# Kernel optimization log

Hardware: AMD Instinct MI355X
Metric: run time of the kernel (lower is better)

## Reference

```python
import jax, jax.numpy as jnp
import numpy as np

B, N, F, T, E, OUT = 16, 5000, 8, 12, 160000, 64


def setup_inputs() -> dict:
    key = jax.random.key(0)
    ks = jax.random.split(key, 20)
    d = {}
    d["x"] = jax.random.normal(ks[0], (B, N, F, T), dtype=jnp.float32)
    d["edge_index"] = jax.random.randint(ks[1], (2, E), 0, N, dtype=jnp.int32)
    def p(k, shape, scale=0.1):
        return jax.random.normal(k, shape, dtype=jnp.float32) * scale
    i = 2
    for g in ("z", "r", "h"):
        d[f"W{g}"] = p(ks[i], (F, OUT)); i += 1        # GCNConv weight
        d[f"b{g}"] = p(ks[i], (OUT,)); i += 1           # GCNConv bias
        d[f"L{g}"] = p(ks[i], (2 * OUT, OUT)); i += 1   # gate Linear weight
        d[f"lb{g}"] = p(ks[i], (OUT,)); i += 1          # gate Linear bias
    d["att"] = p(ks[i], (T,)); i += 1                   # A3TGCN attention logits
    d["fcW"] = p(ks[i], (OUT, T)); i += 1               # final Linear 64->periods
    d["fcb"] = p(ks[i], (T,))
    return d


def _gcn(xs, W, b, src, dst, norm, n_nodes):
    # xs: [M, N, F] -> D^{-1/2}(A+I)D^{-1/2} (xs W) + b
    support = xs @ W                                    # [M, N, OUT]
    msg = support[:, src, :] * norm[None, :, None]      # gather at source
    agg = jax.vmap(lambda m: jax.ops.segment_sum(m, dst, num_segments=n_nodes))(msg)
    return agg + b


def reference(x, edge_index, Wz, bz, Lz, lbz, Wr, br, Lr, lbr, Wh, bh, Lh, lbh, att, fcW, fcb):
    b_sz, n_nodes, _, periods = x.shape
    src, dst = edge_index[0], edge_index[1]
    loop = jnp.arange(n_nodes, dtype=src.dtype)
    src = jnp.concatenate([src, loop])                  # add self loops
    dst = jnp.concatenate([dst, loop])
    deg = jax.ops.segment_sum(jnp.ones(src.shape, jnp.float32), dst, num_segments=n_nodes)
    dinv = jnp.where(deg > 0, jax.lax.rsqrt(deg), 0.0)
    norm = dinv[src] * dinv[dst]                        # symmetric GCN normalization

    # In A3TGCN the hidden state is never carried across periods (stays zero),
    # so all periods are independent: fold T into the batch axis.
    xs = jnp.moveaxis(x, 3, 0).reshape(periods * b_sz, n_nodes, x.shape[2])
    H = jnp.zeros((periods * b_sz, n_nodes, Wz.shape[1]), x.dtype)

    Z = jax.nn.sigmoid(jnp.concatenate([_gcn(xs, Wz, bz, src, dst, norm, n_nodes), H], -1) @ Lz + lbz)
    R = jax.nn.sigmoid(jnp.concatenate([_gcn(xs, Wr, br, src, dst, norm, n_nodes), H], -1) @ Lr + lbr)
    Ht = jnp.tanh(jnp.concatenate([_gcn(xs, Wh, bh, src, dst, norm, n_nodes), H * R], -1) @ Lh + lbh)
    Hnew = Z * H + (1.0 - Z) * Ht                       # [T*B, N, 64]

    Hs = Hnew.reshape(periods, b_sz, n_nodes, -1)
    Hacc = jnp.einsum('t,tbnh->bnh', jax.nn.softmax(att), Hs)
    return Hacc @ fcW + fcb                             # [B, N, periods]
```

## Files before the change

kernel.cpp:

```cpp
#include <hip/hip_runtime.h>

#define NN 5000
#define FF 8
#define TT 12
#define EE 160000
#define HH 64
#define EN (EE + NN)
#define CAP (EN + 7 * NN + 64)
#define XBSTRIDE 1920000
#define BSOFF    15360000

typedef float f2  __attribute__((ext_vector_type(2)));
typedef float f4v __attribute__((ext_vector_type(4)));

#define LOG2E 1.44269504088896340736f


__global__ void k_count(const int* __restrict__ dst, int* __restrict__ deg) {
    int i = blockIdx.x * blockDim.x + threadIdx.x;
    if (i < EE) atomicAdd(&deg[dst[i]], 1);
}

__global__ __launch_bounds__(256) void k_scan_prep(
    const int* __restrict__ deg, int* __restrict__ offs, int* __restrict__ cursor,
    float* __restrict__ dinv,
    const float* __restrict__ Wz, const float* __restrict__ bz,
    const float* __restrict__ Lz, const float* __restrict__ lbz,
    const float* __restrict__ Wh, const float* __restrict__ bh,
    const float* __restrict__ Lh, const float* __restrict__ lbh,
    const float* __restrict__ att,
    float* __restrict__ G, float* __restrict__ C, float* __restrict__ sm) {
    int tid = threadIdx.x;
    if (blockIdx.x == 0) {
        __shared__ int s[256];
        int base = tid * 20;
        int pad[20], real[20];
        int part = 0;
#pragma unroll
        for (int j = 0; j < 20; ++j) {
            int n = base + j;
            int c = (n < NN) ? deg[n] + 1 : 0;
            real[j] = c;
            pad[j] = (c + 7) & ~7;
            part += pad[j];
        }
        s[tid] = part;
        __syncthreads();
        for (int d = 1; d < 256; d <<= 1) {
            int v = (tid >= d) ? s[tid - d] : 0;
            __syncthreads();
            s[tid] += v;
            __syncthreads();
        }
        int run = s[tid] - part;
#pragma unroll
        for (int j = 0; j < 20; ++j) {
            int n = base + j;
            if (n < NN) {
                offs[n] = run;
                cursor[n] = run;
                dinv[n] = rsqrtf((float)real[j]);
                run += pad[j];
            }
        }
        if (tid == 255) offs[NN] = s[255];
    } else {
        for (int idx = tid; idx < 1024; idx += 256) {
            int g = idx >> 9, rem = idx & 511, f = rem >> 6, o = rem & 63;
            const float* W = g ? Wh : Wz;
            const float* L = g ? Lh : Lz;
            float acc = 0.f;
            for (int k = 0; k < 64; ++k) acc += W[f * 64 + k] * L[k * 64 + o];
            G[idx] = acc * (g ? 2.0f * LOG2E : LOG2E);
        }
        for (int idx = tid; idx < 128; idx += 256) {
            int g = idx >> 6, o = idx & 63;
            const float* b = g ? bh : bz;
            const float* L = g ? Lh : Lz;
            const float* lb = g ? lbh : lbz;
            float acc = lb[o];
            for (int k = 0; k < 64; ++k) acc += b[k] * L[k * 64 + o];
            C[idx] = acc * (g ? 2.0f * LOG2E : LOG2E);
        }
        if (tid == 0) {
            float m = att[0];
            for (int t = 1; t < TT; ++t) m = fmaxf(m, att[t]);
            float e[TT], ss = 0.f;
            for (int t = 0; t < TT; ++t) { e[t] = __expf(att[t] - m); ss += e[t]; }
            for (int t = 0; t < TT; ++t) sm[t] = e[t] / ss;
        }
    }
}

__global__ void k_fill(const int* __restrict__ src, const int* __restrict__ dst,
                       int* cursor, const float* __restrict__ dinv,
                       int2* __restrict__ cedge) {
    int i = blockIdx.x * blockDim.x + threadIdx.x;
    if (i < EE) {
        int s = src[i], d = dst[i];
        int p = atomicAdd(&cursor[d], 1);
        cedge[p] = make_int2(s, __float_as_int(dinv[s] * dinv[d]));
    } else if (i < EN) {
        int n = i - EE;
        int p = atomicAdd(&cursor[n], 1);
        cedge[p] = make_int2(n, __float_as_int(dinv[n] * dinv[n]));
    }
}


#define E2(Q)                                                     \
    {                                                             \
        unsigned a0_ = (unsigned)(Q).x * 384u + voff;             \
        unsigned a1_ = (unsigned)(Q).z * 384u + voff;             \
        f4v v0_ = *(const f4v*)(xbb + a0_);                       \
        f4v v1_ = *(const f4v*)(xbb + a1_);                       \
        acc += __int_as_float((Q).y) * v0_;                       \
        acc += __int_as_float((Q).w) * v1_;                       \
    }

__global__ __launch_bounds__(256) void k_fused(
    const float* __restrict__ x, const int* __restrict__ offs,
    const int2* __restrict__ cedge,
    const float* __restrict__ G, const float* __restrict__ C,
    const float* __restrict__ sm, const float* __restrict__ fcW,
    const float* __restrict__ fcb, float* __restrict__ out) {
    __shared__ __align__(16) float xals[4][2][96];
    __shared__ __align__(16) float hl[4][2][72];
    __shared__ __align__(16) float fcw[768];
    __shared__ __align__(16) float Glds[1024];
    __shared__ __align__(16) float Clds[128];

    const int tid = threadIdx.x;
    const int wid = tid >> 6;
    const int lane = tid & 63;
    const int bp = blockIdx.x & 7;
    const int g = blockIdx.x >> 3;
    const int n = g * 4 + wid;

    ((f4v*)Glds)[tid] = ((const f4v*)G)[tid];
    if (tid < 192) ((f4v*)fcw)[tid] = ((const f4v*)fcW)[tid];
    if (tid < 32) ((f4v*)Clds)[tid] = ((const f4v*)C)[tid];

    int r0 = __builtin_amdgcn_readfirstlane(offs[n]);
    int r1 = __builtin_amdgcn_readfirstlane(offs[n + 1]);

    const char* xbb = (const char*)x + (size_t)bp * XBSTRIDE;

    if (lane < 48) {
        const unsigned voff = (unsigned)(lane / 24) * BSOFF + (unsigned)(lane % 24) * 16u;
        f4v acc = {0.f, 0.f, 0.f, 0.f};

        const int4* ce = (const int4*)cedge;
        int c = r0 >> 1;
        const int c1 = r1 >> 1;
        int4 A0 = ce[c], A1 = ce[c + 1], A2 = ce[c + 2], A3 = ce[c + 3];
        int4 B0 = ce[c + 4], B1 = ce[c + 5], B2 = ce[c + 6], B3 = ce[c + 7];
        while (true) {
            int4 D0 = A0, D1 = A1, D2 = A2, D3 = A3;
            A0 = B0; A1 = B1; A2 = B2; A3 = B3;
            B0 = ce[c + 8]; B1 = ce[c + 9]; B2 = ce[c + 10]; B3 = ce[c + 11];
            E2(D0) E2(D1) E2(D2) E2(D3)
            c += 4;
            if (c >= c1) break;
        }
        *(f4v*)&xals[wid][lane / 24][(lane % 24) * 4] = acc;
    }
    __syncthreads();

    float gz[FF], gh[FF];
#pragma unroll
    for (int f = 0; f < FF; ++f) {
        gz[f] = Glds[f * 64 + lane];
        gh[f] = Glds[512 + f * 64 + lane];
    }
    float cz = Clds[lane], ch = Clds[64 + lane];
    float smv[TT];
#pragma unroll
    for (int t = 0; t < TT; ++t) smv[t] = sm[t];

#pragma unroll
    for (int bs = 0; bs < 2; ++bs) {
        float hacc = 0.f;
#pragma unroll
        for (int tq = 0; tq < 3; ++tq) {
            f4v xq[FF];
#pragma unroll
            for (int f = 0; f < FF; ++f)
                xq[f] = *(const f4v*)&xals[wid][bs][f * TT + tq * 4];
#pragma unroll
            for (int half = 0; half < 2; ++half) {
                f2 az = {cz, cz}, ah = {ch, ch};
#pragma unroll
                for (int f = 0; f < FF; ++f) {
                    f2 v = half ? xq[f].hi : xq[f].lo;
                    az += v * gz[f];
                    ah += v * gh[f];
                }
#pragma unroll
                for (int j = 0; j < 2; ++j) {
                    float ea = exp2f(az[j]);
                    float e2h = exp2f(ah[j]);
                    float num = e2h - 1.0f;
                    float den = (1.0f + ea) * (1.0f + e2h);
                    hacc += smv[tq * 4 + half * 2 + j] * num * __builtin_amdgcn_rcpf(den);
                }
            }
        }
        hl[wid][bs][lane] = hacc;
    }
    __syncthreads();

    if (tid < 48) {
        int nw = tid / 12;
        int rem = tid % 12;
        int bs = rem / 6;
        int tp = rem % 6;
        f2 acc;
        acc[0] = fcb[2 * tp];
        acc[1] = fcb[2 * tp + 1];
        const float* hrow = &hl[nw][bs][0];
#pragma unroll
        for (int o4 = 0; o4 < 16; ++o4) {
            f4v h4 = *(const f4v*)&hrow[o4 * 4];
            f2 w0 = *(const f2*)&fcw[(o4 * 4 + 0) * TT + 2 * tp];
            f2 w1 = *(const f2*)&fcw[(o4 * 4 + 1) * TT + 2 * tp];
            f2 w2 = *(const f2*)&fcw[(o4 * 4 + 2) * TT + 2 * tp];
            f2 w3 = *(const f2*)&fcw[(o4 * 4 + 3) * TT + 2 * tp];
            acc += h4[0] * w0;
            acc += h4[1] * w1;
            acc += h4[2] * w2;
            acc += h4[3] * w3;
        }
        int b = bp + bs * 8;
        int nn2 = g * 4 + nw;
        *(f2*)&out[((size_t)b * NN + nn2) * TT + 2 * tp] = acc;
    }
}

extern "C" void kernel_launch(void* const* d_in, const int* in_sizes, int n_in,
                              void* d_out, int out_size, void* d_ws, size_t ws_size,
                              hipStream_t stream) {
    const float* x   = (const float*)d_in[0];
    const int*   ei  = (const int*)d_in[1];
    const float* Wz  = (const float*)d_in[2];
    const float* bz  = (const float*)d_in[3];
    const float* Lz  = (const float*)d_in[4];
    const float* lbz = (const float*)d_in[5];
    const float* Wh  = (const float*)d_in[10];
    const float* bh  = (const float*)d_in[11];
    const float* Lh  = (const float*)d_in[12];
    const float* lbh = (const float*)d_in[13];
    const float* att = (const float*)d_in[14];
    const float* fcW = (const float*)d_in[15];
    const float* fcb = (const float*)d_in[16];
    float* out = (float*)d_out;

    const int* src = ei;
    const int* dst = ei + EE;

    int2*  cedge  = (int2*)d_ws;
    int*   deg    = (int*)(cedge + CAP);
    int*   cursor = deg + NN;
    int*   offs   = cursor + NN;
    float* dinv   = (float*)(offs + NN + 1);
    float* G      = dinv + NN;
    float* C      = G + 1024;
    float* sm     = C + 128;

    (void)hipMemsetAsync(d_ws, 0, (size_t)CAP * 8 + (size_t)NN * 4, stream);
    hipLaunchKernelGGL(k_count, dim3((EE + 255) / 256), dim3(256), 0, stream, dst, deg);
    hipLaunchKernelGGL(k_scan_prep, dim3(2), dim3(256), 0, stream,
                       deg, offs, cursor, dinv,
                       Wz, bz, Lz, lbz, Wh, bh, Lh, lbh, att, G, C, sm);
    hipLaunchKernelGGL(k_fill, dim3((EN + 255) / 256), dim3(256), 0, stream,
                       src, dst, cursor, dinv, cedge);
    hipLaunchKernelGGL(k_fused, dim3(1250 * 8), dim3(256), 0, stream,
                       x, offs, cedge, G, C, sm, fcW, fcb, out);
}
```

Before: 137.5 us.

## Split fused GCN kernel into gather and dense kernels via workspace buffer

```diff
diff --git a/kernel.cpp b/kernel.cpp
--- a/kernel.cpp
+++ b/kernel.cpp
@@ -9,6 +9,7 @@
 #define CAP (EN + 7 * NN + 64)
 #define XBSTRIDE 1920000
 #define BSOFF    15360000
+#define XAFLOATS (8 * NN * 192)
 
 typedef float f2  __attribute__((ext_vector_type(2)));
 typedef float f4v __attribute__((ext_vector_type(4)));
@@ -28,8 +29,9 @@
     const float* __restrict__ Lz, const float* __restrict__ lbz,
     const float* __restrict__ Wh, const float* __restrict__ bh,
     const float* __restrict__ Lh, const float* __restrict__ lbh,
-    const float* __restrict__ att,
-    float* __restrict__ G, float* __restrict__ C, float* __restrict__ sm) {
+    const float* __restrict__ att, const float* __restrict__ fcW,
+    float* __restrict__ G, float* __restrict__ C, float* __restrict__ sm,
+    float* __restrict__ fcwT) {
     int tid = threadIdx.x;
     if (blockIdx.x == 0) {
         __shared__ int s[256];
@@ -81,6 +83,10 @@
             float acc = lb[o];
             for (int k = 0; k < 64; ++k) acc += b[k] * L[k * 64 + o];
             C[idx] = acc * (g ? 2.0f * LOG2E : LOG2E);
+        }
+        for (int idx = tid; idx < 768; idx += 256) {
+            int t = idx >> 6, o = idx & 63;
+            fcwT[idx] = fcW[o * TT + t];
         }
         if (tid == 0) {
             float m = att[0];
@@ -108,6 +114,126 @@
 }
 
 
+#define E2S(Q)                                                    \
+    {                                                             \
+        unsigned a0_ = (unsigned)(Q).x * 384u + voff;             \
+        unsigned a1_ = (unsigned)(Q).z * 384u + voff;             \
+        f4v v0_ = *(const f4v*)(xbb + a0_);                       \
+        f4v v1_ = *(const f4v*)(xbb + a1_);                       \
+        accA += __int_as_float((Q).y) * v0_;                      \
+        accB += __int_as_float((Q).w) * v1_;                      \
+    }
+
+__global__ __launch_bounds__(256) void k_gather(
+    const float* __restrict__ x, const int* __restrict__ offs,
+    const int2* __restrict__ cedge, float* __restrict__ xa) {
+    const int tid = threadIdx.x;
+    const int wid = tid >> 6;
+    const int lane = tid & 63;
+    const int bp = blockIdx.x & 7;
+    const int n = (blockIdx.x >> 3) * 4 + wid;
+
+    int r0 = __builtin_amdgcn_readfirstlane(offs[n]);
+    int r1 = __builtin_amdgcn_readfirstlane(offs[n + 1]);
+
+    const char* xbb = (const char*)x + (size_t)bp * XBSTRIDE;
+
+    if (lane < 48) {
+        const unsigned voff = (unsigned)(lane / 24) * BSOFF + (unsigned)(lane % 24) * 16u;
+        f4v accA = {0.f, 0.f, 0.f, 0.f};
+        f4v accB = {0.f, 0.f, 0.f, 0.f};
+
+        const int4* ce = (const int4*)cedge;
+        int c = r0 >> 1;
+        const int c1 = r1 >> 1;
+        int4 A0 = ce[c], A1 = ce[c + 1], A2 = ce[c + 2], A3 = ce[c + 3];
+        int4 B0 = ce[c + 4], B1 = ce[c + 5], B2 = ce[c + 6], B3 = ce[c + 7];
+        while (true) {
+            int4 D0 = A0, D1 = A1, D2 = A2, D3 = A3;
+            A0 = B0; A1 = B1; A2 = B2; A3 = B3;
+            B0 = ce[c + 8]; B1 = ce[c + 9]; B2 = ce[c + 10]; B3 = ce[c + 11];
+            E2S(D0) E2S(D1) E2S(D2) E2S(D3)
+            c += 4;
+            if (c >= c1) break;
+        }
+        f4v acc = accA + accB;
+        *(f4v*)(xa + ((size_t)(bp * NN + n)) * 192 + (lane / 24) * 96 + (lane % 24) * 4) = acc;
+    }
+}
+
+
+__global__ __launch_bounds__(256) void k_dense(
+    const float* __restrict__ xa, const float* __restrict__ G,
+    const float* __restrict__ C, const float* __restrict__ sm,
+    const float* __restrict__ fcwT, const float* __restrict__ fcb,
+    float* __restrict__ out) {
+    __shared__ __align__(16) float hl[4][128];
+    const int tid = threadIdx.x;
+    const int wid = tid >> 6;
+    const int lane = tid & 63;
+    const int bp = blockIdx.x & 7;
+    const int n = (blockIdx.x >> 3) * 4 + wid;
+
+    const float* row = xa + ((size_t)(bp * NN + n)) * 192;
+
+    float gz[FF], gh[FF];
+#pragma unroll
+    for (int f = 0; f < FF; ++f) {
+        gz[f] = G[f * 64 + lane];
+        gh[f] = G[512 + f * 64 + lane];
+    }
+    float cz = C[lane], ch = C[64 + lane];
+    float smv[TT];
+#pragma unroll
+    for (int t = 0; t < TT; ++t) smv[t] = sm[t];
+
+#pragma unroll
+    for (int bs = 0; bs < 2; ++bs) {
+        float hacc = 0.f;
+#pragma unroll
+        for (int tq = 0; tq < 3; ++tq) {
+            f4v xq[FF];
+#pragma unroll
+            for (int f = 0; f < FF; ++f)
+                xq[f] = *(const f4v*)(row + bs * 96 + f * TT + tq * 4);
+#pragma unroll
+            for (int half = 0; half < 2; ++half) {
+                f2 az = {cz, cz}, ah = {ch, ch};
+#pragma unroll
+                for (int f = 0; f < FF; ++f) {
+                    f2 v = half ? xq[f].hi : xq[f].lo;
+                    az += v * gz[f];
+                    ah += v * gh[f];
+                }
+#pragma unroll
+                for (int j = 0; j < 2; ++j) {
+                    float ea = exp2f(az[j]);
+                    float e2h = exp2f(ah[j]);
+                    float num = e2h - 1.0f;
+                    float den = (1.0f + ea) * (1.0f + e2h);
+                    hacc += smv[tq * 4 + half * 2 + j] * num * __builtin_amdgcn_rcpf(den);
+                }
+            }
+        }
+        hl[wid][bs * 64 + lane] = hacc;
+    }
+    __syncthreads();
+
+    if (lane < 24) {
+        int bs = lane / 12, t = lane % 12;
+        float acc = fcb[t];
+#pragma unroll
+        for (int o4 = 0; o4 < 16; ++o4) {
+            f4v h4 = *(const f4v*)&hl[wid][bs * 64 + o4 * 4];
+            f4v w4 = *(const f4v*)&fcwT[t * 64 + o4 * 4];
+            acc += h4[0] * w4[0] + h4[1] * w4[1] + h4[2] * w4[2] + h4[3] * w4[3];
+        }
+        int b = bp + bs * 8;
+        out[((size_t)b * NN + n) * TT + t] = acc;
+    }
+}
+
+
 #define E2(Q)                                                     \
     {                                                             \
         unsigned a0_ = (unsigned)(Q).x * 384u + voff;             \
@@ -143,13 +269,11 @@
 
     int r0 = __builtin_amdgcn_readfirstlane(offs[n]);
     int r1 = __builtin_amdgcn_readfirstlane(offs[n + 1]);
-
     const char* xbb = (const char*)x + (size_t)bp * XBSTRIDE;
 
     if (lane < 48) {
         const unsigned voff = (unsigned)(lane / 24) * BSOFF + (unsigned)(lane % 24) * 16u;
         f4v acc = {0.f, 0.f, 0.f, 0.f};
-
         const int4* ce = (const int4*)cedge;
         int c = r0 >> 1;
         const int c1 = r1 >> 1;
@@ -258,7 +382,13 @@
     const int* src = ei;
     const int* dst = ei + EE;
 
-    int2*  cedge  = (int2*)d_ws;
+    const size_t need = (size_t)XAFLOATS * 4 + (size_t)CAP * 8 +
+                        (size_t)(3 * NN + 1) * 4 + (size_t)NN * 4 +
+                        (1024 + 128 + 16 + 768) * 4;
+    const bool split = ws_size >= need;
+
+    float* xa     = (float*)d_ws;
+    int2*  cedge  = split ? (int2*)(xa + XAFLOATS) : (int2*)d_ws;
     int*   deg    = (int*)(cedge + CAP);
     int*   cursor = deg + NN;
     int*   offs   = cursor + NN;
@@ -266,14 +396,22 @@
     float* G      = dinv + NN;
     float* C      = G + 1024;
     float* sm     = C + 128;
-
-    (void)hipMemsetAsync(d_ws, 0, (size_t)CAP * 8 + (size_t)NN * 4, stream);
+    float* fcwT   = sm + 16;
+
+    (void)hipMemsetAsync(cedge, 0, (size_t)CAP * 8 + (size_t)NN * 4, stream);
     hipLaunchKernelGGL(k_count, dim3((EE + 255) / 256), dim3(256), 0, stream, dst, deg);
     hipLaunchKernelGGL(k_scan_prep, dim3(2), dim3(256), 0, stream,
                        deg, offs, cursor, dinv,
-                       Wz, bz, Lz, lbz, Wh, bh, Lh, lbh, att, G, C, sm);
+                       Wz, bz, Lz, lbz, Wh, bh, Lh, lbh, att, fcW, G, C, sm, fcwT);
     hipLaunchKernelGGL(k_fill, dim3((EN + 255) / 256), dim3(256), 0, stream,
                        src, dst, cursor, dinv, cedge);
-    hipLaunchKernelGGL(k_fused, dim3(1250 * 8), dim3(256), 0, stream,
-                       x, offs, cedge, G, C, sm, fcW, fcb, out);
-}
+    if (split) {
+        hipLaunchKernelGGL(k_gather, dim3(1250 * 8), dim3(256), 0, stream,
+                           x, offs, cedge, xa);
+        hipLaunchKernelGGL(k_dense, dim3(1250 * 8), dim3(256), 0, stream,
+                           xa, G, C, sm, fcwT, fcb, out);
+    } else {
+        hipLaunchKernelGGL(k_fused, dim3(1250 * 8), dim3(256), 0, stream,
+                           x, offs, cedge, G, C, sm, fcW, fcb, out);
+    }
+}
```

Result: slower. 195.7 us (+42.4%).

## Use one 64-thread block per node, split accumulators, pretranspose fc weights

Applied to the files above, without the earlier changes.

```diff
diff --git a/kernel.cpp b/kernel.cpp
--- a/kernel.cpp
+++ b/kernel.cpp
@@ -21,23 +21,24 @@
     if (i < EE) atomicAdd(&deg[dst[i]], 1);
 }
 
-__global__ __launch_bounds__(256) void k_scan_prep(
+__global__ __launch_bounds__(1024) void k_scan_prep(
     const int* __restrict__ deg, int* __restrict__ offs, int* __restrict__ cursor,
     float* __restrict__ dinv,
     const float* __restrict__ Wz, const float* __restrict__ bz,
     const float* __restrict__ Lz, const float* __restrict__ lbz,
     const float* __restrict__ Wh, const float* __restrict__ bh,
     const float* __restrict__ Lh, const float* __restrict__ lbh,
-    const float* __restrict__ att,
-    float* __restrict__ G, float* __restrict__ C, float* __restrict__ sm) {
+    const float* __restrict__ att, const float* __restrict__ fcW,
+    float* __restrict__ G, float* __restrict__ C, float* __restrict__ sm,
+    float* __restrict__ fcwT) {
     int tid = threadIdx.x;
     if (blockIdx.x == 0) {
-        __shared__ int s[256];
-        int base = tid * 20;
-        int pad[20], real[20];
+        __shared__ int s[1024];
+        int base = tid * 5;
+        int pad[5], real[5];
         int part = 0;
 #pragma unroll
-        for (int j = 0; j < 20; ++j) {
+        for (int j = 0; j < 5; ++j) {
             int n = base + j;
             int c = (n < NN) ? deg[n] + 1 : 0;
             real[j] = c;
@@ -46,7 +47,7 @@
         }
         s[tid] = part;
         __syncthreads();
-        for (int d = 1; d < 256; d <<= 1) {
+        for (int d = 1; d < 1024; d <<= 1) {
             int v = (tid >= d) ? s[tid - d] : 0;
             __syncthreads();
             s[tid] += v;
@@ -54,7 +55,7 @@
         }
         int run = s[tid] - part;
 #pragma unroll
-        for (int j = 0; j < 20; ++j) {
+        for (int j = 0; j < 5; ++j) {
             int n = base + j;
             if (n < NN) {
                 offs[n] = run;
@@ -63,24 +64,28 @@
                 run += pad[j];
             }
         }
-        if (tid == 255) offs[NN] = s[255];
+        if (tid == 1023) offs[NN] = s[1023];
     } else {
-        for (int idx = tid; idx < 1024; idx += 256) {
-            int g = idx >> 9, rem = idx & 511, f = rem >> 6, o = rem & 63;
+        if (tid < 1024) {
+            int g = tid >> 9, rem = tid & 511, f = rem >> 6, o = rem & 63;
             const float* W = g ? Wh : Wz;
             const float* L = g ? Lh : Lz;
             float acc = 0.f;
             for (int k = 0; k < 64; ++k) acc += W[f * 64 + k] * L[k * 64 + o];
-            G[idx] = acc * (g ? 2.0f * LOG2E : LOG2E);
-        }
-        for (int idx = tid; idx < 128; idx += 256) {
-            int g = idx >> 6, o = idx & 63;
+            G[tid] = acc * (g ? 2.0f * LOG2E : LOG2E);
+        }
+        if (tid < 128) {
+            int g = tid >> 6, o = tid & 63;
             const float* b = g ? bh : bz;
             const float* L = g ? Lh : Lz;
             const float* lb = g ? lbh : lbz;
             float acc = lb[o];
             for (int k = 0; k < 64; ++k) acc += b[k] * L[k * 64 + o];
-            C[idx] = acc * (g ? 2.0f * LOG2E : LOG2E);
+            C[tid] = acc * (g ? 2.0f * LOG2E : LOG2E);
+        }
+        if (tid < 768) {
+            int t = tid >> 6, o = tid & 63;
+            fcwT[tid] = fcW[o * TT + t];
         }
         if (tid == 0) {
             float m = att[0];
@@ -108,38 +113,28 @@
 }
 
 
-#define E2(Q)                                                     \
+#define E2S(Q)                                                    \
     {                                                             \
         unsigned a0_ = (unsigned)(Q).x * 384u + voff;             \
         unsigned a1_ = (unsigned)(Q).z * 384u + voff;             \
         f4v v0_ = *(const f4v*)(xbb + a0_);                       \
         f4v v1_ = *(const f4v*)(xbb + a1_);                       \
-        acc += __int_as_float((Q).y) * v0_;                       \
-        acc += __int_as_float((Q).w) * v1_;                       \
-    }
-
-__global__ __launch_bounds__(256) void k_fused(
+        accA += __int_as_float((Q).y) * v0_;                      \
+        accB += __int_as_float((Q).w) * v1_;                      \
+    }
+
+__global__ __launch_bounds__(64) void k_node(
     const float* __restrict__ x, const int* __restrict__ offs,
     const int2* __restrict__ cedge,
     const float* __restrict__ G, const float* __restrict__ C,
-    const float* __restrict__ sm, const float* __restrict__ fcW,
+    const float* __restrict__ sm, const float* __restrict__ fcwT,
     const float* __restrict__ fcb, float* __restrict__ out) {
-    __shared__ __align__(16) float xals[4][2][96];
-    __shared__ __align__(16) float hl[4][2][72];
-    __shared__ __align__(16) float fcw[768];
-    __shared__ __align__(16) float Glds[1024];
-    __shared__ __align__(16) float Clds[128];
-
-    const int tid = threadIdx.x;
-    const int wid = tid >> 6;
-    const int lane = tid & 63;
+    __shared__ __align__(16) float xals[2][96];
+    __shared__ __align__(16) float hl[2][64];
+
+    const int lane = threadIdx.x;
     const int bp = blockIdx.x & 7;
-    const int g = blockIdx.x >> 3;
-    const int n = g * 4 + wid;
-
-    ((f4v*)Glds)[tid] = ((const f4v*)G)[tid];
-    if (tid < 192) ((f4v*)fcw)[tid] = ((const f4v*)fcW)[tid];
-    if (tid < 32) ((f4v*)Clds)[tid] = ((const f4v*)C)[tid];
+    const int n = blockIdx.x >> 3;
 
     int r0 = __builtin_amdgcn_readfirstlane(offs[n]);
     int r1 = __builtin_amdgcn_readfirstlane(offs[n + 1]);
@@ -148,7 +143,8 @@
 
     if (lane < 48) {
         const unsigned voff = (unsigned)(lane / 24) * BSOFF + (unsigned)(lane % 24) * 16u;
-        f4v acc = {0.f, 0.f, 0.f, 0.f};
+        f4v accA = {0.f, 0.f, 0.f, 0.f};
+        f4v accB = {0.f, 0.f, 0.f, 0.f};
 
         const int4* ce = (const int4*)cedge;
         int c = r0 >> 1;
@@ -159,21 +155,22 @@
             int4 D0 = A0, D1 = A1, D2 = A2, D3 = A3;
             A0 = B0; A1 = B1; A2 = B2; A3 = B3;
             B0 = ce[c + 8]; B1 = ce[c + 9]; B2 = ce[c + 10]; B3 = ce[c + 11];
-            E2(D0) E2(D1) E2(D2) E2(D3)
+            E2S(D0) E2S(D1) E2S(D2) E2S(D3)
             c += 4;
             if (c >= c1) break;
         }
-        *(f4v*)&xals[wid][lane / 24][(lane % 24) * 4] = acc;
+        f4v acc = accA + accB;
+        *(f4v*)&xals[lane / 24][(lane % 24) * 4] = acc;
     }
     __syncthreads();
 
     float gz[FF], gh[FF];
 #pragma unroll
     for (int f = 0; f < FF; ++f) {
-        gz[f] = Glds[f * 64 + lane];
-        gh[f] = Glds[512 + f * 64 + lane];
-    }
-    float cz = Clds[lane], ch = Clds[64 + lane];
+        gz[f] = G[f * 64 + lane];
+        gh[f] = G[512 + f * 64 + lane];
+    }
+    float cz = C[lane], ch = C[64 + lane];
     float smv[TT];
 #pragma unroll
     for (int t = 0; t < TT; ++t) smv[t] = sm[t];
@@ -186,7 +183,7 @@
             f4v xq[FF];
 #pragma unroll
             for (int f = 0; f < FF; ++f)
-                xq[f] = *(const f4v*)&xals[wid][bs][f * TT + tq * 4];
+                xq[f] = *(const f4v*)&xals[bs][f * TT + tq * 4];
 #pragma unroll
             for (int half = 0; half < 2; ++half) {
                 f2 az = {cz, cz}, ah = {ch, ch};
@@ -206,34 +203,21 @@
                 }
             }
         }
-        hl[wid][bs][lane] = hacc;
+        hl[bs][lane] = hacc;
     }
     __syncthreads();
 
-    if (tid < 48) {
-        int nw = tid / 12;
-        int rem = tid % 12;
-        int bs = rem / 6;
-        int tp = rem % 6;
-        f2 acc;
-        acc[0] = fcb[2 * tp];
-        acc[1] = fcb[2 * tp + 1];
-        const float* hrow = &hl[nw][bs][0];
+    if (lane < 24) {
+        int bs = lane / 12, t = lane % 12;
+        float acc = fcb[t];
 #pragma unroll
         for (int o4 = 0; o4 < 16; ++o4) {
-            f4v h4 = *(const f4v*)&hrow[o4 * 4];
-            f2 w0 = *(const f2*)&fcw[(o4 * 4 + 0) * TT + 2 * tp];
-            f2 w1 = *(const f2*)&fcw[(o4 * 4 + 1) * TT + 2 * tp];
-            f2 w2 = *(const f2*)&fcw[(o4 * 4 + 2) * TT + 2 * tp];
-            f2 w3 = *(const f2*)&fcw[(o4 * 4 + 3) * TT + 2 * tp];
-            acc += h4[0] * w0;
-            acc += h4[1] * w1;
-            acc += h4[2] * w2;
-            acc += h4[3] * w3;
+            f4v h4 = *(const f4v*)&hl[bs][o4 * 4];
+            f4v w4 = *(const f4v*)&fcwT[t * 64 + o4 * 4];
+            acc += h4[0] * w4[0] + h4[1] * w4[1] + h4[2] * w4[2] + h4[3] * w4[3];
         }
         int b = bp + bs * 8;
-        int nn2 = g * 4 + nw;
-        *(f2*)&out[((size_t)b * NN + nn2) * TT + 2 * tp] = acc;
+        out[((size_t)b * NN + n) * TT + t] = acc;
     }
 }
 
@@ -266,14 +250,15 @@
     float* G      = dinv + NN;
     float* C      = G + 1024;
     float* sm     = C + 128;
+    float* fcwT   = sm + 16;
 
     (void)hipMemsetAsync(d_ws, 0, (size_t)CAP * 8 + (size_t)NN * 4, stream);
     hipLaunchKernelGGL(k_count, dim3((EE + 255) / 256), dim3(256), 0, stream, dst, deg);
-    hipLaunchKernelGGL(k_scan_prep, dim3(2), dim3(256), 0, stream,
+    hipLaunchKernelGGL(k_scan_prep, dim3(2), dim3(1024), 0, stream,
                        deg, offs, cursor, dinv,
-                       Wz, bz, Lz, lbz, Wh, bh, Lh, lbh, att, G, C, sm);
+                       Wz, bz, Lz, lbz, Wh, bh, Lh, lbh, att, fcW, G, C, sm, fcwT);
     hipLaunchKernelGGL(k_fill, dim3((EN + 255) / 256), dim3(256), 0, stream,
                        src, dst, cursor, dinv, cedge);
-    hipLaunchKernelGGL(k_fused, dim3(1250 * 8), dim3(256), 0, stream,
-                       x, offs, cedge, G, C, sm, fcW, fcb, out);
-}
+    hipLaunchKernelGGL(k_node, dim3(NN * 8), dim3(64), 0, stream,
+                       x, offs, cedge, G, C, sm, fcwT, fcb, out);
+}
```

Result: faster. 133.7 us (-2.7%).
